# Kernel optimization log

Hardware: AMD Instinct MI355X
Metric: run time of the kernel (lower is better)

## Reference

```python
import jax, jax.numpy as jnp
import numpy as np

SR = 22050
N_MELS = 128
N_FFT = 2048
HOP = 512


def _mel_filterbank(sr, n_fft, n_mels):
    """librosa slaney-scale, slaney-normalized mel filterbank [n_mels, 1+n_fft//2]."""
    f_sp = 200.0 / 3
    min_log_hz = 1000.0
    min_log_mel = min_log_hz / f_sp
    logstep = np.log(6.4) / 27.0

    def hz_to_mel(f):
        f = np.asarray(f, dtype=np.float64)
        return np.where(f >= min_log_hz,
                        min_log_mel + np.log(np.maximum(f, min_log_hz) / min_log_hz) / logstep,
                        f / f_sp)

    def mel_to_hz(m):
        m = np.asarray(m, dtype=np.float64)
        return np.where(m >= min_log_mel,
                        min_log_hz * np.exp(logstep * (m - min_log_mel)),
                        f_sp * m)

    fmax = sr / 2.0
    fftfreqs = np.linspace(0.0, sr / 2.0, 1 + n_fft // 2)
    mel_f = mel_to_hz(np.linspace(hz_to_mel(0.0), hz_to_mel(fmax), n_mels + 2))
    fdiff = np.diff(mel_f)
    ramps = mel_f[:, None] - fftfreqs[None, :]
    lower = -ramps[:-2] / fdiff[:-1, None]
    upper = ramps[2:] / fdiff[1:, None]
    weights = np.maximum(0.0, np.minimum(lower, upper))
    enorm = 2.0 / (mel_f[2:n_mels + 2] - mel_f[:n_mels])  # slaney norm
    weights *= enorm[:, None]
    return weights.astype(np.float32)


def setup_inputs() -> dict:
    key = jax.random.key(0)
    x = jax.random.normal(key, (8, 661500, 2), dtype=jnp.float32) * 0.1
    mel_fb = jnp.asarray(_mel_filterbank(SR, N_FFT, N_MELS))  # [n_mels, 1+n_fft//2]
    return {"x": x, "mel_fb": mel_fb}


def reference(x, mel_fb):
    # x: (B, S, C) -> (B, n_mels, T, C), power-2 mel spectrogram (librosa defaults)
    y = jnp.transpose(x, (0, 2, 1))  # (B, C, S)
    pad = N_FFT // 2
    y = jnp.pad(y, ((0, 0), (0, 0), (pad, pad)), mode='reflect')
    n_frames = 1 + (y.shape[-1] - N_FFT) // HOP
    n = jnp.arange(N_FFT)
    # periodic hann window (scipy get_window('hann', N, fftbins=True))
    window = (0.5 - 0.5 * jnp.cos(2.0 * jnp.pi * n / N_FFT)).astype(x.dtype)
    idx = jnp.arange(n_frames)[:, None] * HOP + n[None, :]  # (T, n_fft)
    frames = y[:, :, idx] * window  # (B, C, T, n_fft)
    spec = jnp.fft.rfft(frames, axis=-1)  # (B, C, T, 1+n_fft//2)
    power = spec.real ** 2 + spec.imag ** 2  # |STFT|^2
    mel = jnp.einsum('mf,bctf->bmtc', mel_fb, power)  # (B, n_mels, T, C)
    return mel
```

## Files before the change

kernel.cpp:

```cpp
#include <hip/hip_runtime.h>
#include <math.h>

#define N_MELS   128
#define N_FFT    2048
#define HOP      512
#define BATCH    8
#define S_LEN    661500
#define CH       2
#define T_FRAMES 1292
#define NBINS    1025

#define ANG 0.003067961575771282f

#define WS_WIN     0
#define WS_TW      8192
#define WS_WBEG    24576
#define WS_WN4     25088
#define WS_WTAB    25600

#define PW_OFF   1060
#define PW_FR    2120

#define ZN 2304

typedef float vf2 __attribute__((ext_vector_type(2)));

__device__ __forceinline__ vf2 cadd(vf2 a, vf2 b){ return a + b; }
__device__ __forceinline__ vf2 csub(vf2 a, vf2 b){ return a - b; }
__device__ __forceinline__ vf2 cnegi(vf2 z){ return (vf2){ z.y, -z.x }; }
__device__ __forceinline__ vf2 cmul(vf2 a, vf2 b){
    vf2 t = a.yy * b.yx;
    vf2 s = (vf2){ -t.x, t.y };
    return a.xx * b + s;
}

__device__ __forceinline__ void bfly8(const vf2* a, vf2* b) {
    const float C = 0.70710678118654752f;
    vf2 e0=a[0]+a[4], e1=a[1]+a[5], e2=a[2]+a[6], e3=a[3]+a[7];
    vf2 o0=a[0]-a[4], o1=a[1]-a[5], o2=a[2]-a[6], o3=a[3]-a[7];
    vf2 t1 = (o1 + cnegi(o1)) * C;
    vf2 t2 = cnegi(o2);
    vf2 t3 = (cnegi(o3) - o3) * C;
    {
        vf2 s0=e0+e2, d0=e0-e2;
        vf2 s1=e1+e3, d1=e1-e3;
        b[0]=s0+s1; b[4]=s0-s1;
        vf2 nd1=cnegi(d1);
        b[2]=d0+nd1; b[6]=d0-nd1;
    }
    {
        vf2 s0=o0+t2, d0=o0-t2;
        vf2 s1=t1+t3, d1=t1-t3;
        b[1]=s0+s1; b[5]=s0-s1;
        vf2 nd1=cnegi(d1);
        b[3]=d0+nd1; b[7]=d0-nd1;
    }
}

__device__ __forceinline__ void stage_pair(vf2* rA, vf2* rB, vf2 w1) {
    vf2 bqA[8], bqB[8];
    bfly8(rA, bqA);
    bfly8(rB, bqB);
    vf2 w2 = cmul(w1, w1);
    vf2 w3 = cmul(w2, w1);
    vf2 w4 = cmul(w2, w2);
    vf2 w5 = cmul(w4, w1);
    vf2 w6 = cmul(w4, w2);
    vf2 w7 = cmul(w4, w3);
    rA[0] = bqA[0];           rB[0] = bqB[0];
    rA[1] = cmul(w1, bqA[1]); rB[1] = cmul(w1, bqB[1]);
    rA[2] = cmul(w2, bqA[2]); rB[2] = cmul(w2, bqB[2]);
    rA[3] = cmul(w3, bqA[3]); rB[3] = cmul(w3, bqB[3]);
    rA[4] = cmul(w4, bqA[4]); rB[4] = cmul(w4, bqB[4]);
    rA[5] = cmul(w5, bqA[5]); rB[5] = cmul(w5, bqB[5]);
    rA[6] = cmul(w6, bqA[6]); rB[6] = cmul(w6, bqB[6]);
    rA[7] = cmul(w7, bqA[7]); rB[7] = cmul(w7, bqB[7]);
}

__device__ __forceinline__ void bf4(const vf2* I, vf2* O) {
    vf2 apc=I[0]+I[2], amc=I[0]-I[2];
    vf2 bpd=I[1]+I[3], bmd=I[1]-I[3];
    vf2 nb = cnegi(bmd);
    O[0]=apc+bpd; O[1]=amc+nb;
    O[2]=apc-bpd; O[3]=amc-nb;
}

__device__ __forceinline__ vf2 upair(vf2 Zf, vf2 Zm) {
    vf2 B = (vf2){ Zm.x, -Zm.y };
    vf2 e = Zf + B;
    vf2 d = Zf - B;
    vf2 ee = e * e;
    vf2 dd = d * d;
    return (vf2){ 0.25f*(ee.x + ee.y), 0.25f*(dd.x + dd.y) };
}

__global__ __launch_bounds__(256) void setup_kernel(
        const float* __restrict__ fb, float* __restrict__ ws) {
    int blk = blockIdx.x;
    if (blk < 8) {
        int i = blk * 256 + threadIdx.x;
        float*  win = ws;
        float2* tw  = (float2*)((char*)ws + WS_TW);
        win[i] = 0.5f - 0.5f * cosf(ANG * (float)i);
        float sn, cs; sincosf(-ANG * (float)i, &sn, &cs);
        tw[i] = make_float2(cs, sn);
    } else {
        int m = blk - 8;
        int lane = threadIdx.x;
        if (lane < 64) {
            int*   wbeg = (int*)((char*)ws + WS_WBEG);
            int*   wn4  = (int*)((char*)ws + WS_WN4);
            float* wtab = (float*)((char*)ws + WS_WTAB);
            const float* row = fb + m * NBINS;
            int s = NBINS;
            int e = 0;
            for (int f = lane; f < NBINS; f += 64) {
                if (row[f] != 0.0f) { if (f < s) s = f; if (f > e) e = f; }
            }
            #pragma unroll
            for (int o = 32; o; o >>= 1) {
                s = min(s, __shfl_xor(s, o));
                e = max(e, __shfl_xor(e, o));
            }
            int a0 = s & ~3;
            if (a0 > NBINS - 1) a0 = (NBINS - 1) & ~3;
            int n4 = (e - a0 + 4) >> 2;
            if (n4 < 1) n4 = 1;
            if (n4 > 16) n4 = 16;
            if (lane == 0) { wbeg[m] = a0; wn4[m] = n4; }
            int f = a0 + lane;
            wtab[(m << 6) + lane] = (f < NBINS) ? row[f] : 0.0f;
        }
    }
}

__global__ __launch_bounds__(256, 8) void mel_spec_kernel(
        const float* __restrict__ x, const float* __restrict__ fb,
        const float* __restrict__ ws, float* __restrict__ out) {
    __shared__ float4 Zq[ZN/2];
    vf2*   Z2  = (vf2*)Zq;
    float* pwb = (float*)Zq;

    const float* win  = ws;
    const vf2*   tw   = (const vf2*)((const char*)ws + WS_TW);
    const int*   wbeg = (const int*)((const char*)ws + WS_WBEG);
    const int*   wn4  = (const int*)((const char*)ws + WS_WN4);
    const float* wtab = (const float*)((const char*)ws + WS_WTAB);

    const int tid = threadIdx.x;
    const int bid = blockIdx.x;
    const int b   = bid & 7;
    const int t0  = (bid >> 3) * 2;

    const vf2* xb = (const vf2*)x + (size_t)b * S_LEN;
    const int tbA = t0*HOP - (N_FFT/2);
    const int tbB = tbA + HOP;

    vf2 rA[8], rB[8];
    const int rb = tid + 2*(tid>>4);

    if (tbA >= 0 && tbB + (N_FFT - 1) < S_LEN) {
        vf2 v[10];
        #pragma unroll
        for (int k = 0; k < 10; ++k) v[k] = xb[tbA + tid + 256*k];
        #pragma unroll
        for (int k = 0; k < 8; ++k) {
            float w = win[tid + 256*k];
            rA[k] = v[k]   * w;
            rB[k] = v[k+2] * w;
        }
    } else {
        #pragma unroll
        for (int k = 0; k < 8; ++k) {
            int n  = tid + 256*k;
            float w = win[n];
            int sA = tbA + n;
            if (sA < 0) sA = -sA; else if (sA >= S_LEN) sA = 2*S_LEN - 2 - sA;
            rA[k] = xb[sA] * w;
            int sB = tbB + n;
            if (sB < 0) sB = -sB; else if (sB >= S_LEN) sB = 2*S_LEN - 2 - sB;
            rB[k] = xb[sB] * w;
        }
    }

    stage_pair(rA, rB, tw[tid]);
    {
        const int f4 = 4*tid + (tid>>1);
        #pragma unroll
        for (int j = 0; j < 4; ++j)
            Zq[f4+j] = make_float4(rA[2*j].x, rA[2*j].y, rA[2*j+1].x, rA[2*j+1].y);
        __syncthreads();
        #pragma unroll
        for (int k = 0; k < 8; ++k) rA[k] = Z2[rb + 288*k];
        __syncthreads();
        #pragma unroll
        for (int j = 0; j < 4; ++j)
            Zq[f4+j] = make_float4(rB[2*j].x, rB[2*j].y, rB[2*j+1].x, rB[2*j+1].y);
        __syncthreads();
        #pragma unroll
        for (int k = 0; k < 8; ++k) rB[k] = Z2[rb + 288*k];
        __syncthreads();
    }

    stage_pair(rA, rB, tw[tid & ~7]);
    {
        const int base = (tid & 7) + 72*(tid >> 3);
        #pragma unroll
        for (int k = 0; k < 8; ++k) Z2[base + 8*k + 2*(k>>1)] = rA[k];
        __syncthreads();
        #pragma unroll
        for (int k = 0; k < 8; ++k) rA[k] = Z2[rb + 288*k];
        __syncthreads();
        #pragma unroll
        for (int k = 0; k < 8; ++k) Z2[base + 8*k + 2*(k>>1)] = rB[k];
        __syncthreads();
        #pragma unroll
        for (int k = 0; k < 8; ++k) rB[k] = Z2[rb + 288*k];
        __syncthreads();
    }

    stage_pair(rA, rB, tw[tid & ~63]);
    const int b2  = (tid == 0) ? 256 : 512 - tid;
    const int rb2 = b2 + 2*(b2>>4);
    vf2 A1[4], A2[4], B1[4], B2[4];
    {
        const int q = tid & 63;
        const int base = q + 2*(q>>4) + 576*(tid >> 6);
        #pragma unroll
        for (int k = 0; k < 8; ++k) Z2[base + 72*k] = rA[k];
        __syncthreads();
        #pragma unroll
        for (int k = 0; k < 4; ++k) { A1[k] = Z2[rb + 576*k]; A2[k] = Z2[rb2 + 576*k]; }
        __syncthreads();
        #pragma unroll
        for (int k = 0; k < 8; ++k) Z2[base + 72*k] = rB[k];
        __syncthreads();
        #pragma unroll
        for (int k = 0; k < 4; ++k) { B1[k] = Z2[rb + 576*k]; B2[k] = Z2[rb2 + 576*k]; }
        __syncthreads();
    }

    if (tid < 140) {
        int p = tid / 35;
        int o = tid - p * 35;
        pwb[(p>>1)*PW_FR + (p&1)*PW_OFF + 1025 + o] = 0.0f;
    }
    {
        vf2 O1[4], O2[4];
        bf4(A1, O1); bf4(A2, O2);
        float* pwf = pwb;
        if (tid == 0) {
            vf2 p;
            p = upair(O1[0], O1[0]); pwf[0]    = p.x; pwf[PW_OFF+0]    = p.y;
            p = upair(O1[1], O1[3]); pwf[512]  = p.x; pwf[PW_OFF+512]  = p.y;
            p = upair(O1[2], O1[2]); pwf[1024] = p.x; pwf[PW_OFF+1024] = p.y;
            p = upair(O2[0], O2[3]); pwf[256]  = p.x; pwf[PW_OFF+256]  = p.y;
            p = upair(O2[1], O2[2]); pwf[768]  = p.x; pwf[PW_OFF+768]  = p.y;
        } else {
            vf2 p;
            p = upair(O1[0], O2[3]); pwf[tid]      = p.x; pwf[PW_OFF+tid]      = p.y;
            p = upair(O1[1], O2[2]); pwf[tid+512]  = p.x; pwf[PW_OFF+tid+512]  = p.y;
            p = upair(O2[0], O1[3]); pwf[512-tid]  = p.x; pwf[PW_OFF+512-tid]  = p.y;
            p = upair(O2[1], O1[2]); pwf[1024-tid] = p.x; pwf[PW_OFF+1024-tid] = p.y;
        }
    }
    {
        vf2 O1[4], O2[4];
        bf4(B1, O1); bf4(B2, O2);
        float* pwf = pwb + PW_FR;
        if (tid == 0) {
            vf2 p;
            p = upair(O1[0], O1[0]); pwf[0]    = p.x; pwf[PW_OFF+0]    = p.y;
            p = upair(O1[1], O1[3]); pwf[512]  = p.x; pwf[PW_OFF+512]  = p.y;
            p = upair(O1[2], O1[2]); pwf[1024] = p.x; pwf[PW_OFF+1024] = p.y;
            p = upair(O2[0], O2[3]); pwf[256]  = p.x; pwf[PW_OFF+256]  = p.y;
            p = upair(O2[1], O2[2]); pwf[768]  = p.x; pwf[PW_OFF+768]  = p.y;
        } else {
            vf2 p;
            p = upair(O1[0], O2[3]); pwf[tid]      = p.x; pwf[PW_OFF+tid]      = p.y;
            p = upair(O1[1], O2[2]); pwf[tid+512]  = p.x; pwf[PW_OFF+tid+512]  = p.y;
            p = upair(O2[0], O1[3]); pwf[512-tid]  = p.x; pwf[PW_OFF+512-tid]  = p.y;
            p = upair(O2[1], O1[2]); pwf[1024-tid] = p.x; pwf[PW_OFF+1024-tid] = p.y;
        }
    }
    __syncthreads();

    {
        int m  = tid >> 1;
        int h  = tid & 1;
        int a0 = wbeg[m];
        int n4 = wn4[m];
        const float4* wt4 = (const float4*)(wtab + (m << 6));
        const float4* q0  = (const float4*)(pwb + h*PW_FR + a0);
        const float4* q1  = (const float4*)(pwb + h*PW_FR + PW_OFF + a0);
        vf2 acc0 = (vf2){0.0f, 0.0f};
        vf2 acc1 = (vf2){0.0f, 0.0f};
        for (int j = 0; j < n4; ++j) {
            float4 w4 = wt4[j];
            float4 r0 = q0[j];
            float4 r1 = q1[j];
            vf2 wlo = (vf2){w4.x, w4.y}, whi = (vf2){w4.z, w4.w};
            acc0 += wlo * (vf2){r0.x, r0.y};
            acc0 += whi * (vf2){r0.z, r0.w};
            acc1 += wlo * (vf2){r1.x, r1.y};
            acc1 += whi * (vf2){r1.z, r1.w};
        }
        size_t base = (((size_t)b * N_MELS + m) * T_FRAMES + t0 + h) * CH;
        *(float2*)(out + base) = make_float2(acc0.x + acc0.y, acc1.x + acc1.y);
    }
}

extern "C" void kernel_launch(void* const* d_in, const int* in_sizes, int n_in,
                              void* d_out, int out_size, void* d_ws, size_t ws_size,
                              hipStream_t stream) {
    const float* x  = (const float*)d_in[0];
    const float* fb = (const float*)d_in[1];
    float* out = (float*)d_out;
    float* ws  = (float*)d_ws;

    setup_kernel<<<8 + N_MELS, 256, 0, stream>>>(fb, ws);
    mel_spec_kernel<<<BATCH * (T_FRAMES/2), 256, 0, stream>>>(x, fb, ws, out);
}
```

Before: 120.5 us.

## Process four frames per 512-thread block and load twiddles from table

The mel kernel now uses 512-thread blocks, each handling four frames. Two 256-thread halves each run a 2048-point FFT on their own shared-memory region, two frames in sequence, and the mel projection uses four threads per mel row. Twiddle powers are read from the precomputed table instead of being built by repeated complex multiplies, and the window values are loaded once per thread. The setup kernel packs four mel rows per block. This reduces per-block overhead and register pressure, but the FFT frames now run one after another inside each half, and the blocks are larger with twice the shared memory.

```diff
diff --git a/kernel.cpp b/kernel.cpp
--- a/kernel.cpp
+++ b/kernel.cpp
@@ -21,12 +21,10 @@
 #define PW_OFF   1060
 #define PW_FR    2120
 
-#define ZN 2304
+#define ZF4 1152
 
 typedef float vf2 __attribute__((ext_vector_type(2)));
 
-__device__ __forceinline__ vf2 cadd(vf2 a, vf2 b){ return a + b; }
-__device__ __forceinline__ vf2 csub(vf2 a, vf2 b){ return a - b; }
 __device__ __forceinline__ vf2 cnegi(vf2 z){ return (vf2){ z.y, -z.x }; }
 __device__ __forceinline__ vf2 cmul(vf2 a, vf2 b){
     vf2 t = a.yy * b.yx;
@@ -57,24 +55,15 @@
     }
 }
 
-__device__ __forceinline__ void stage_pair(vf2* rA, vf2* rB, vf2 w1) {
-    vf2 bqA[8], bqB[8];
-    bfly8(rA, bqA);
-    bfly8(rB, bqB);
-    vf2 w2 = cmul(w1, w1);
-    vf2 w3 = cmul(w2, w1);
-    vf2 w4 = cmul(w2, w2);
-    vf2 w5 = cmul(w4, w1);
-    vf2 w6 = cmul(w4, w2);
-    vf2 w7 = cmul(w4, w3);
-    rA[0] = bqA[0];           rB[0] = bqB[0];
-    rA[1] = cmul(w1, bqA[1]); rB[1] = cmul(w1, bqB[1]);
-    rA[2] = cmul(w2, bqA[2]); rB[2] = cmul(w2, bqB[2]);
-    rA[3] = cmul(w3, bqA[3]); rB[3] = cmul(w3, bqB[3]);
-    rA[4] = cmul(w4, bqA[4]); rB[4] = cmul(w4, bqB[4]);
-    rA[5] = cmul(w5, bqA[5]); rB[5] = cmul(w5, bqB[5]);
-    rA[6] = cmul(w6, bqA[6]); rB[6] = cmul(w6, bqB[6]);
-    rA[7] = cmul(w7, bqA[7]); rB[7] = cmul(w7, bqB[7]);
+__device__ __forceinline__ void stage_tw(vf2* r, const vf2* tw, int tb) {
+    vf2 tws[7];
+    #pragma unroll
+    for (int j = 0; j < 7; ++j) tws[j] = tw[(j+1)*tb];
+    vf2 bq[8];
+    bfly8(r, bq);
+    r[0] = bq[0];
+    #pragma unroll
+    for (int j = 0; j < 7; ++j) r[j+1] = cmul(tws[j], bq[j+1]);
 }
 
 __device__ __forceinline__ void bf4(const vf2* I, vf2* O) {
@@ -94,51 +83,64 @@
     return (vf2){ 0.25f*(ee.x + ee.y), 0.25f*(dd.x + dd.y) };
 }
 
+__device__ __forceinline__ void store_frame(float* pwf, int lt, const vf2* p)
+{
+    if (lt == 0) {
+        pwf[0]    = p[0].x; pwf[PW_OFF+0]    = p[0].y;
+        pwf[512]  = p[1].x; pwf[PW_OFF+512]  = p[1].y;
+        pwf[1024] = p[2].x; pwf[PW_OFF+1024] = p[2].y;
+        pwf[256]  = p[3].x; pwf[PW_OFF+256]  = p[3].y;
+        pwf[768]  = p[4].x; pwf[PW_OFF+768]  = p[4].y;
+    } else {
+        pwf[lt]      = p[0].x; pwf[PW_OFF+lt]      = p[0].y;
+        pwf[lt+512]  = p[1].x; pwf[PW_OFF+lt+512]  = p[1].y;
+        pwf[512-lt]  = p[2].x; pwf[PW_OFF+512-lt]  = p[2].y;
+        pwf[1024-lt] = p[3].x; pwf[PW_OFF+1024-lt] = p[3].y;
+    }
+}
+
 __global__ __launch_bounds__(256) void setup_kernel(
         const float* __restrict__ fb, float* __restrict__ ws) {
     int blk = blockIdx.x;
-    if (blk < 8) {
-        int i = blk * 256 + threadIdx.x;
+    if (blk >= 32) {
+        int i = (blk - 32) * 256 + threadIdx.x;
         float*  win = ws;
         float2* tw  = (float2*)((char*)ws + WS_TW);
         win[i] = 0.5f - 0.5f * cosf(ANG * (float)i);
         float sn, cs; sincosf(-ANG * (float)i, &sn, &cs);
         tw[i] = make_float2(cs, sn);
     } else {
-        int m = blk - 8;
-        int lane = threadIdx.x;
-        if (lane < 64) {
-            int*   wbeg = (int*)((char*)ws + WS_WBEG);
-            int*   wn4  = (int*)((char*)ws + WS_WN4);
-            float* wtab = (float*)((char*)ws + WS_WTAB);
-            const float* row = fb + m * NBINS;
-            int s = NBINS;
-            int e = 0;
-            for (int f = lane; f < NBINS; f += 64) {
-                if (row[f] != 0.0f) { if (f < s) s = f; if (f > e) e = f; }
-            }
-            #pragma unroll
-            for (int o = 32; o; o >>= 1) {
-                s = min(s, __shfl_xor(s, o));
-                e = max(e, __shfl_xor(e, o));
-            }
-            int a0 = s & ~3;
-            if (a0 > NBINS - 1) a0 = (NBINS - 1) & ~3;
-            int n4 = (e - a0 + 4) >> 2;
-            if (n4 < 1) n4 = 1;
-            if (n4 > 16) n4 = 16;
-            if (lane == 0) { wbeg[m] = a0; wn4[m] = n4; }
-            int f = a0 + lane;
-            wtab[(m << 6) + lane] = (f < NBINS) ? row[f] : 0.0f;
-        }
-    }
-}
-
-__global__ __launch_bounds__(256, 8) void mel_spec_kernel(
+        int m    = blk * 4 + (threadIdx.x >> 6);
+        int lane = threadIdx.x & 63;
+        int*   wbeg = (int*)((char*)ws + WS_WBEG);
+        int*   wn4  = (int*)((char*)ws + WS_WN4);
+        float* wtab = (float*)((char*)ws + WS_WTAB);
+        const float* row = fb + m * NBINS;
+        int s = NBINS;
+        int e = 0;
+        for (int f = lane; f < NBINS; f += 64) {
+            if (row[f] != 0.0f) { if (f < s) s = f; if (f > e) e = f; }
+        }
+        #pragma unroll
+        for (int o = 32; o; o >>= 1) {
+            s = min(s, __shfl_xor(s, o));
+            e = max(e, __shfl_xor(e, o));
+        }
+        int a0 = s & ~3;
+        if (a0 > NBINS - 1) a0 = (NBINS - 1) & ~3;
+        int n4 = (e - a0 + 4) >> 2;
+        if (n4 < 1) n4 = 1;
+        if (n4 > 16) n4 = 16;
+        if (lane == 0) { wbeg[m] = a0; wn4[m] = n4; }
+        int f = a0 + lane;
+        wtab[(m << 6) + lane] = (f < NBINS) ? row[f] : 0.0f;
+    }
+}
+
+__global__ __launch_bounds__(512, 8) void mel_spec_kernel(
         const float* __restrict__ x, const float* __restrict__ fb,
         const float* __restrict__ ws, float* __restrict__ out) {
-    __shared__ float4 Zq[ZN/2];
-    vf2*   Z2  = (vf2*)Zq;
+    __shared__ float4 Zq[2*ZF4];
     float* pwb = (float*)Zq;
 
     const float* win  = ws;
@@ -148,146 +150,101 @@
     const float* wtab = (const float*)((const char*)ws + WS_WTAB);
 
     const int tid = threadIdx.x;
+    const int lt  = tid & 255;
+    const int fh  = tid >> 8;
     const int bid = blockIdx.x;
     const int b   = bid & 7;
-    const int t0  = (bid >> 3) * 2;
+    const int t0  = (bid >> 3) * 4;
+
+    float4* Zqh = Zq + fh * ZF4;
+    vf2*    Z2h = (vf2*)Zqh;
 
     const vf2* xb = (const vf2*)x + (size_t)b * S_LEN;
-    const int tbA = t0*HOP - (N_FFT/2);
-    const int tbB = tbA + HOP;
-
-    vf2 rA[8], rB[8];
-    const int rb = tid + 2*(tid>>4);
-
-    if (tbA >= 0 && tbB + (N_FFT - 1) < S_LEN) {
-        vf2 v[10];
-        #pragma unroll
-        for (int k = 0; k < 10; ++k) v[k] = xb[tbA + tid + 256*k];
-        #pragma unroll
-        for (int k = 0; k < 8; ++k) {
-            float w = win[tid + 256*k];
-            rA[k] = v[k]   * w;
-            rB[k] = v[k+2] * w;
-        }
-    } else {
-        #pragma unroll
-        for (int k = 0; k < 8; ++k) {
-            int n  = tid + 256*k;
-            float w = win[n];
-            int sA = tbA + n;
-            if (sA < 0) sA = -sA; else if (sA >= S_LEN) sA = 2*S_LEN - 2 - sA;
-            rA[k] = xb[sA] * w;
-            int sB = tbB + n;
-            if (sB < 0) sB = -sB; else if (sB >= S_LEN) sB = 2*S_LEN - 2 - sB;
-            rB[k] = xb[sB] * w;
-        }
-    }
-
-    stage_pair(rA, rB, tw[tid]);
+
+    const int rb    = lt + 2*(lt>>4);
+    const int b2    = (lt == 0) ? 256 : 512 - lt;
+    const int rb2   = b2 + 2*(b2>>4);
+    const int f4    = 4*lt + (lt>>1);
+    const int base2 = (lt & 7) + 72*(lt >> 3);
+    const int q3    = lt & 63;
+    const int base3 = q3 + 2*(q3>>4) + 576*(lt >> 6);
+    const int tb1   = lt;
+    const int tb2   = lt & ~7;
+    const int tb3   = lt & ~63;
+
+    float wv[8];
+    #pragma unroll
+    for (int k = 0; k < 8; ++k) wv[k] = win[lt + 256*k];
+
+    auto do_frame = [&](int fr, vf2* pout) {
+        const int tb = fr*HOP - (N_FFT/2);
+        vf2 r[8];
+        if (tb >= 0 && tb + (N_FFT - 1) < S_LEN) {
+            #pragma unroll
+            for (int k = 0; k < 8; ++k) r[k] = xb[tb + lt + 256*k] * wv[k];
+        } else {
+            #pragma unroll
+            for (int k = 0; k < 8; ++k) {
+                int s = tb + lt + 256*k;
+                if (s < 0) s = -s; else if (s >= S_LEN) s = 2*S_LEN - 2 - s;
+                r[k] = xb[s] * wv[k];
+            }
+        }
+        stage_tw(r, tw, tb1);
+        #pragma unroll
+        for (int j = 0; j < 4; ++j)
+            Zqh[f4+j] = make_float4(r[2*j].x, r[2*j].y, r[2*j+1].x, r[2*j+1].y);
+        __syncthreads();
+        #pragma unroll
+        for (int k = 0; k < 8; ++k) r[k] = Z2h[rb + 288*k];
+        __syncthreads();
+        stage_tw(r, tw, tb2);
+        #pragma unroll
+        for (int k = 0; k < 8; ++k) Z2h[base2 + 8*k + 2*(k>>1)] = r[k];
+        __syncthreads();
+        #pragma unroll
+        for (int k = 0; k < 8; ++k) r[k] = Z2h[rb + 288*k];
+        __syncthreads();
+        stage_tw(r, tw, tb3);
+        #pragma unroll
+        for (int k = 0; k < 8; ++k) Z2h[base3 + 72*k] = r[k];
+        __syncthreads();
+        vf2 F1[4], F2[4];
+        #pragma unroll
+        for (int k = 0; k < 4; ++k) { F1[k] = Z2h[rb + 576*k]; F2[k] = Z2h[rb2 + 576*k]; }
+        __syncthreads();
+        vf2 O1[4], O2[4];
+        bf4(F1, O1); bf4(F2, O2);
+        if (lt == 0) {
+            pout[0] = upair(O1[0], O1[0]);
+            pout[1] = upair(O1[1], O1[3]);
+            pout[2] = upair(O1[2], O1[2]);
+            pout[3] = upair(O2[0], O2[3]);
+            pout[4] = upair(O2[1], O2[2]);
+        } else {
+            pout[0] = upair(O1[0], O2[3]);
+            pout[1] = upair(O1[1], O2[2]);
+            pout[2] = upair(O2[0], O1[3]);
+            pout[3] = upair(O2[1], O1[2]);
+            pout[4] = (vf2){0.0f, 0.0f};
+        }
+    };
+
+    vf2 p0[5], p1[5];
+    do_frame(t0 + fh,     p0);
+    do_frame(t0 + 2 + fh, p1);
+
+    store_frame(pwb + fh*PW_FR,     lt, p0);
+    store_frame(pwb + (2+fh)*PW_FR, lt, p1);
+    if (tid < 280) {
+        int pl = tid / 35, o = tid - pl*35;
+        pwb[(pl>>1)*PW_FR + (pl&1)*PW_OFF + 1025 + o] = 0.0f;
+    }
+    __syncthreads();
+
     {
-        const int f4 = 4*tid + (tid>>1);
-        #pragma unroll
-        for (int j = 0; j < 4; ++j)
-            Zq[f4+j] = make_float4(rA[2*j].x, rA[2*j].y, rA[2*j+1].x, rA[2*j+1].y);
-        __syncthreads();
-        #pragma unroll
-        for (int k = 0; k < 8; ++k) rA[k] = Z2[rb + 288*k];
-        __syncthreads();
-        #pragma unroll
-        for (int j = 0; j < 4; ++j)
-            Zq[f4+j] = make_float4(rB[2*j].x, rB[2*j].y, rB[2*j+1].x, rB[2*j+1].y);
-        __syncthreads();
-        #pragma unroll
-        for (int k = 0; k < 8; ++k) rB[k] = Z2[rb + 288*k];
-        __syncthreads();
-    }
-
-    stage_pair(rA, rB, tw[tid & ~7]);
-    {
-        const int base = (tid & 7) + 72*(tid >> 3);
-        #pragma unroll
-        for (int k = 0; k < 8; ++k) Z2[base + 8*k + 2*(k>>1)] = rA[k];
-        __syncthreads();
-        #pragma unroll
-        for (int k = 0; k < 8; ++k) rA[k] = Z2[rb + 288*k];
-        __syncthreads();
-        #pragma unroll
-        for (int k = 0; k < 8; ++k) Z2[base + 8*k + 2*(k>>1)] = rB[k];
-        __syncthreads();
-        #pragma unroll
-        for (int k = 0; k < 8; ++k) rB[k] = Z2[rb + 288*k];
-        __syncthreads();
-    }
-
-    stage_pair(rA, rB, tw[tid & ~63]);
-    const int b2  = (tid == 0) ? 256 : 512 - tid;
-    const int rb2 = b2 + 2*(b2>>4);
-    vf2 A1[4], A2[4], B1[4], B2[4];
-    {
-        const int q = tid & 63;
-        const int base = q + 2*(q>>4) + 576*(tid >> 6);
-        #pragma unroll
-        for (int k = 0; k < 8; ++k) Z2[base + 72*k] = rA[k];
-        __syncthreads();
-        #pragma unroll
-        for (int k = 0; k < 4; ++k) { A1[k] = Z2[rb + 576*k]; A2[k] = Z2[rb2 + 576*k]; }
-        __syncthreads();
-        #pragma unroll
-        for (int k = 0; k < 8; ++k) Z2[base + 72*k] = rB[k];
-        __syncthreads();
-        #pragma unroll
-        for (int k = 0; k < 4; ++k) { B1[k] = Z2[rb + 576*k]; B2[k] = Z2[rb2 + 576*k]; }
-        __syncthreads();
-    }
-
-    if (tid < 140) {
-        int p = tid / 35;
-        int o = tid - p * 35;
-        pwb[(p>>1)*PW_FR + (p&1)*PW_OFF + 1025 + o] = 0.0f;
-    }
-    {
-        vf2 O1[4], O2[4];
-        bf4(A1, O1); bf4(A2, O2);
-        float* pwf = pwb;
-        if (tid == 0) {
-            vf2 p;
-            p = upair(O1[0], O1[0]); pwf[0]    = p.x; pwf[PW_OFF+0]    = p.y;
-            p = upair(O1[1], O1[3]); pwf[512]  = p.x; pwf[PW_OFF+512]  = p.y;
-            p = upair(O1[2], O1[2]); pwf[1024] = p.x; pwf[PW_OFF+1024] = p.y;
-            p = upair(O2[0], O2[3]); pwf[256]  = p.x; pwf[PW_OFF+256]  = p.y;
-            p = upair(O2[1], O2[2]); pwf[768]  = p.x; pwf[PW_OFF+768]  = p.y;
-        } else {
-            vf2 p;
-            p = upair(O1[0], O2[3]); pwf[tid]      = p.x; pwf[PW_OFF+tid]      = p.y;
-            p = upair(O1[1], O2[2]); pwf[tid+512]  = p.x; pwf[PW_OFF+tid+512]  = p.y;
-            p = upair(O2[0], O1[3]); pwf[512-tid]  = p.x; pwf[PW_OFF+512-tid]  = p.y;
-            p = upair(O2[1], O1[2]); pwf[1024-tid] = p.x; pwf[PW_OFF+1024-tid] = p.y;
-        }
-    }
-    {
-        vf2 O1[4], O2[4];
-        bf4(B1, O1); bf4(B2, O2);
-        float* pwf = pwb + PW_FR;
-        if (tid == 0) {
-            vf2 p;
-            p = upair(O1[0], O1[0]); pwf[0]    = p.x; pwf[PW_OFF+0]    = p.y;
-            p = upair(O1[1], O1[3]); pwf[512]  = p.x; pwf[PW_OFF+512]  = p.y;
-            p = upair(O1[2], O1[2]); pwf[1024] = p.x; pwf[PW_OFF+1024] = p.y;
-            p = upair(O2[0], O2[3]); pwf[256]  = p.x; pwf[PW_OFF+256]  = p.y;
-            p = upair(O2[1], O2[2]); pwf[768]  = p.x; pwf[PW_OFF+768]  = p.y;
-        } else {
-            vf2 p;
-            p = upair(O1[0], O2[3]); pwf[tid]      = p.x; pwf[PW_OFF+tid]      = p.y;
-            p = upair(O1[1], O2[2]); pwf[tid+512]  = p.x; pwf[PW_OFF+tid+512]  = p.y;
-            p = upair(O2[0], O1[3]); pwf[512-tid]  = p.x; pwf[PW_OFF+512-tid]  = p.y;
-            p = upair(O2[1], O1[2]); pwf[1024-tid] = p.x; pwf[PW_OFF+1024-tid] = p.y;
-        }
-    }
-    __syncthreads();
-
-    {
-        int m  = tid >> 1;
-        int h  = tid & 1;
+        int m  = tid >> 2;
+        int h  = tid & 3;
         int a0 = wbeg[m];
         int n4 = wn4[m];
         const float4* wt4 = (const float4*)(wtab + (m << 6));
@@ -318,6 +275,6 @@
     float* out = (float*)d_out;
     float* ws  = (float*)d_ws;
 
-    setup_kernel<<<8 + N_MELS, 256, 0, stream>>>(fb, ws);
-    mel_spec_kernel<<<BATCH * (T_FRAMES/2), 256, 0, stream>>>(x, fb, ws, out);
-}
+    setup_kernel<<<40, 256, 0, stream>>>(fb, ws);
+    mel_spec_kernel<<<BATCH * (T_FRAMES/4), 512, 0, stream>>>(x, fb, ws, out);
+}
```

After: 272.0 us. 2.26x slower.
